# Kernel tuning notes

Measured on AMD Instinct MI355X. Metric: run time of the kernel, lower is better.

Reference implementation:

```python
import jax, jax.numpy as jnp
import numpy as np

C = 512
NH = 4
HD = C // NH
G = 32  # min(32, C) and C % 32 == 0
EPS = 1e-5


def setup_inputs() -> dict:
    key = jax.random.key(0)
    ks = jax.random.split(key, 11)
    s = 1.0 / np.sqrt(C)
    return {
        "x": jax.random.normal(ks[0], (16, C, 32, 32), dtype=jnp.float32),
        "gamma": jnp.ones((C,), jnp.float32),
        "beta": jnp.zeros((C,), jnp.float32),
        "wq": jax.random.normal(ks[1], (C, C), jnp.float32) * s,
        "bq": jax.random.normal(ks[2], (C,), jnp.float32) * 0.01,
        "wk": jax.random.normal(ks[3], (C, C), jnp.float32) * s,
        "bk": jax.random.normal(ks[4], (C,), jnp.float32) * 0.01,
        "wv": jax.random.normal(ks[5], (C, C), jnp.float32) * s,
        "bv": jax.random.normal(ks[6], (C,), jnp.float32) * 0.01,
        "wp": jax.random.normal(ks[7], (C, C), jnp.float32) * s,
        "bp": jax.random.normal(ks[8], (C,), jnp.float32) * 0.01,
    }


def _group_norm(x, gamma, beta):
    b, c, h, w = x.shape
    xr = x.reshape(b, G, c // G, h, w)
    mean = xr.mean(axis=(2, 3, 4), keepdims=True)
    var = xr.var(axis=(2, 3, 4), keepdims=True)
    xn = ((xr - mean) * jax.lax.rsqrt(var + EPS)).reshape(b, c, h, w)
    return xn * gamma[None, :, None, None] + beta[None, :, None, None]


def _conv1x1(x, w, b):
    # 1x1 conv == per-position channel GEMM
    return jnp.einsum('oc,bchw->bohw', w, x) + b[None, :, None, None]


def reference(x, gamma, beta, wq, bq, wk, bk, wv, bv, wp, bp):
    b, c, h, w = x.shape
    hw = h * w
    scale = HD ** (-0.5)
    hn = _group_norm(x, gamma, beta)
    q = _conv1x1(hn, wq, bq).reshape(b, NH, HD, hw)
    k = _conv1x1(hn, wk, bk).reshape(b, NH, HD, hw)
    v = _conv1x1(hn, wv, bv).reshape(b, NH, HD, hw)
    attn = jnp.einsum('bhdq,bhdk->bhqk', q, k) * scale  # [b, nh, hw, hw]
    attn = jax.nn.softmax(attn, axis=-1)
    out = jnp.einsum('bhqk,bhdk->bhdq', attn, v)  # [b, nh, hd, hw]
    out = out.reshape(b, c, h, w)
    out = _conv1x1(out, wp, bp)
    return x + out
```

## Files before the change

### kernel.cpp

```cpp
#include <hip/hip_runtime.h>
#include <math.h>

#define CCH 512
#define NH 4
#define HD 128
#define HW 1024
#define BATCH 16
#define EPS 1e-5f

typedef __attribute__((ext_vector_type(8))) short bfrag;
typedef __attribute__((ext_vector_type(4))) float f4;
typedef __attribute__((ext_vector_type(16))) float f16v;

static __device__ __forceinline__ unsigned short f2bf(float f) {
  union { float f; unsigned u; } v;
  v.f = f;
  unsigned r = v.u + 0x7fff + ((v.u >> 16) & 1);
  return (unsigned short)(r >> 16);
}
static __device__ __forceinline__ unsigned pack2(unsigned short a, unsigned short b) {
  return (unsigned)a | ((unsigned)b << 16);
}
static __device__ __forceinline__ void ldg_lds16(const unsigned short* g,
                                                 unsigned short* l) {
  __builtin_amdgcn_global_load_lds(
      (const __attribute__((address_space(1))) unsigned int*)g,
      (__attribute__((address_space(3))) unsigned int*)l, 16, 0, 0);
}

#define QSCALE 0.08838834764831845f

__global__ __launch_bounds__(256) void wcvt_kernel(const float* __restrict__ s0,
                                                   const float* __restrict__ s1,
                                                   const float* __restrict__ s2,
                                                   const float* __restrict__ s3,
                                                   unsigned short* __restrict__ d) {
  const float* srcs[4] = {s0, s1, s2, s3};
  const float* s = srcs[blockIdx.y];
  unsigned short* dp = d + (size_t)blockIdx.y * CCH * CCH;
  int i = blockIdx.x * 256 + threadIdx.x;
  f4 v = ((const f4*)s)[i];
  ushort4 o;
  o.x = f2bf(v.x); o.y = f2bf(v.y); o.z = f2bf(v.z); o.w = f2bf(v.w);
  ((ushort4*)dp)[i] = o;
}

__global__ __launch_bounds__(256) void gn_kernel(const float* __restrict__ x,
                                                 const float* __restrict__ gamma,
                                                 const float* __restrict__ beta,
                                                 unsigned short* __restrict__ hn) {
  int b = blockIdx.x >> 5, g = blockIdx.x & 31;
  const float* xp = x + ((size_t)b * CCH + g * 16) * HW;
  int t = threadIdx.x;
  float s = 0.f, ss = 0.f;
  const f4* xp4 = (const f4*)xp;
  for (int i = t; i < 4096; i += 256) {
    f4 v = xp4[i];
    s += v.x + v.y + v.z + v.w;
    ss += v.x * v.x + v.y * v.y + v.z * v.z + v.w * v.w;
  }
#pragma unroll
  for (int off = 32; off > 0; off >>= 1) {
    s += __shfl_xor(s, off);
    ss += __shfl_xor(ss, off);
  }
  __shared__ float rs[4], rss[4];
  int w = t >> 6;
  if ((t & 63) == 0) { rs[w] = s; rss[w] = ss; }
  __syncthreads();
  s = rs[0] + rs[1] + rs[2] + rs[3];
  ss = rss[0] + rss[1] + rss[2] + rss[3];
  const float invn = 1.f / (16 * HW);
  float mean = s * invn;
  float var = ss * invn - mean * mean;
  float rstd = rsqrtf(var + EPS);
  float a_[16], b_[16];
#pragma unroll
  for (int c = 0; c < 16; ++c) {
    float gm = gamma[g * 16 + c] * rstd;
    a_[c] = gm;
    b_[c] = beta[g * 16 + c] - mean * gm;
  }
#pragma unroll
  for (int i = 0; i < 4; ++i) {
    int p = t + 256 * i;
    unsigned short tv[16];
#pragma unroll
    for (int c = 0; c < 16; ++c) tv[c] = f2bf(xp[c * HW + p] * a_[c] + b_[c]);
    uint4 u0, u1;
    u0.x = pack2(tv[0], tv[1]);  u0.y = pack2(tv[2], tv[3]);
    u0.z = pack2(tv[4], tv[5]);  u0.w = pack2(tv[6], tv[7]);
    u1.x = pack2(tv[8], tv[9]);  u1.y = pack2(tv[10], tv[11]);
    u1.z = pack2(tv[12], tv[13]); u1.w = pack2(tv[14], tv[15]);
    unsigned short* dst = hn + ((size_t)b * HW + p) * CCH + g * 16;
    *(uint4*)dst = u0;
    *(uint4*)(dst + 8) = u1;
  }
}

template <int PROJ>
__global__ __launch_bounds__(256, 3) void mm_kernel(
    const unsigned short* __restrict__ Xt, const unsigned short* __restrict__ Wb,
    const float* __restrict__ b0, const float* __restrict__ b1,
    const float* __restrict__ b2, const float* __restrict__ resid,
    unsigned short* __restrict__ O0, unsigned short* __restrict__ O1,
    unsigned short* __restrict__ O2, float* __restrict__ Ofp) {
  int b = blockIdx.z;
  int p0 = blockIdx.x * 128;
  int c0g = blockIdx.y * 128;
  __shared__ __align__(16) unsigned short Xs[128 * 32];
  __shared__ __align__(16) unsigned short Ws[128 * 32];
  int t = threadIdx.x;
  int w = t >> 6, lane = t & 63, l15 = lane & 15, quad = lane >> 4;
  int wp = (w & 1) * 64, wc = (w >> 1) * 64;
  const unsigned short* Xb = Xt + (size_t)b * HW * CCH;
  const unsigned short* Wr = Wb + (size_t)c0g * CCH;
  f4 acc[4][4] = {};
  for (int k0 = 0; k0 < CCH; k0 += 32) {
    __syncthreads();
#pragma unroll
    for (int j = 0; j < 2; ++j) {
      int chk = w * 2 + j;
      int r = chk * 16 + (lane >> 2);
      int c = (lane & 3) ^ (r & 3);
      ldg_lds16(&Xb[(size_t)(p0 + r) * CCH + k0 + c * 8], &Xs[chk * 512]);
      ldg_lds16(&Wr[(size_t)r * CCH + k0 + c * 8], &Ws[chk * 512]);
    }
    __syncthreads();
    bfrag af[4], bf[4];
#pragma unroll
    for (int pt = 0; pt < 4; ++pt) {
      int r = wp + pt * 16 + l15;
      af[pt] = *(const bfrag*)&Xs[r * 32 + (quad ^ (r & 3)) * 8];
    }
#pragma unroll
    for (int ct = 0; ct < 4; ++ct) {
      int r = wc + ct * 16 + l15;
      bf[ct] = *(const bfrag*)&Ws[r * 32 + (quad ^ (r & 3)) * 8];
    }
#pragma unroll
    for (int pt = 0; pt < 4; ++pt)
#pragma unroll
      for (int ct = 0; ct < 4; ++ct)
        acc[pt][ct] = __builtin_amdgcn_mfma_f32_16x16x32_bf16(
            af[pt], bf[ct], acc[pt][ct], 0, 0, 0);
  }
  if (PROJ) {
#pragma unroll
    for (int ct = 0; ct < 4; ++ct) {
      int ch = c0g + wc + ct * 16 + l15;
      float bi = b0[ch];
#pragma unroll
      for (int pt = 0; pt < 4; ++pt) {
        int pos = p0 + wp + pt * 16 + quad * 4;
        f4 v = acc[pt][ct];
        size_t off = (size_t)b * CCH * HW + (size_t)ch * HW + pos;
        float4 rv = *(const float4*)&resid[off];
        float4 st;
        st.x = v.x + bi + rv.x; st.y = v.y + bi + rv.y;
        st.z = v.z + bi + rv.z; st.w = v.w + bi + rv.w;
        *(float4*)&Ofp[off] = st;
      }
    }
  } else {
    int mat = c0g >> 9;
    int c0 = c0g & 511;
    const float* bias = mat == 0 ? b0 : (mat == 1 ? b1 : b2);
    unsigned short* O = mat == 0 ? O0 : (mat == 1 ? O1 : O2);
    const float sc = (mat == 0) ? QSCALE : 1.0f;
#pragma unroll
    for (int ct = 0; ct < 4; ++ct) {
      int ch = c0 + wc + ct * 16 + l15;
      float bi = bias[ch];
#pragma unroll
      for (int pt = 0; pt < 4; ++pt) {
        int pos = p0 + wp + pt * 16 + quad * 4;
        f4 v = acc[pt][ct];
        if (mat < 2) {
          unsigned short* Op = O + (size_t)b * HW * CCH;
          Op[(size_t)(pos + 0) * CCH + ch] = f2bf((v.x + bi) * sc);
          Op[(size_t)(pos + 1) * CCH + ch] = f2bf((v.y + bi) * sc);
          Op[(size_t)(pos + 2) * CCH + ch] = f2bf((v.z + bi) * sc);
          Op[(size_t)(pos + 3) * CCH + ch] = f2bf((v.w + bi) * sc);
        } else {
          unsigned short* Op = O + (size_t)b * CCH * HW;
          ushort4 st;
          st.x = f2bf(v.x + bi); st.y = f2bf(v.y + bi);
          st.z = f2bf(v.z + bi); st.w = f2bf(v.w + bi);
          *(ushort4*)&Op[(size_t)ch * HW + pos] = st;
        }
      }
    }
  }
}

__global__ __launch_bounds__(512, 2) void attn_kernel(
    const unsigned short* __restrict__ Qt, const unsigned short* __restrict__ Kt,
    const unsigned short* __restrict__ Vc, unsigned short* __restrict__ Ot) {
  int bh = blockIdx.x;
  int b = bh >> 2, h = bh & 3;
  int q0 = blockIdx.y * 256;
  int t = threadIdx.x;
  int w = t >> 6, lane = t & 63;
  int l31 = lane & 31, half = lane >> 5;
  __shared__ __align__(16) unsigned short Ks[2][64 * 128];
  __shared__ __align__(16) unsigned short Vs[2][128 * 64];
  int q = q0 + w * 32 + l31;
  const unsigned short* Kbase = Kt + (size_t)b * HW * CCH + h * HD;
  const unsigned short* Vbase = Vc + ((size_t)b * CCH + h * HD) * HW;
  bfrag qf[8];
#pragma unroll
  for (int ks = 0; ks < 8; ++ks)
    qf[ks] = *(const bfrag*)&Qt[((size_t)b * HW + q) * CCH + h * HD +
                                ks * 16 + half * 8];
  f16v o[4] = {};
  float lrow = 0.f;
  auto stage = [&](int kt, int bi) {
    int kk0 = kt * 64;
#pragma unroll
    for (int j = 0; j < 2; ++j) {
      int chk = w * 2 + j;
      {
        int r = chk * 4 + (lane >> 4);
        int c = (lane & 15) ^ (r & 15);
        ldg_lds16(&Kbase[(size_t)(kk0 + r) * CCH + c * 8], &Ks[bi][chk * 512]);
      }
      {
        int r = chk * 8 + (lane >> 3);
        int c = (lane & 7) ^ (r & 7);
        ldg_lds16(&Vbase[(size_t)r * HW + kk0 + c * 8], &Vs[bi][chk * 512]);
      }
    }
  };
  stage(0, 0);
  for (int kt = 0; kt < 16; ++kt) {
    __syncthreads();
    if (kt < 15) stage(kt + 1, (kt + 1) & 1);
    const unsigned short* K_ = Ks[kt & 1];
    const unsigned short* V_ = Vs[kt & 1];
    f16v S[2] = {};
#pragma unroll
    for (int ks = 0; ks < 8; ++ks) {
      int c16 = ks * 2 + half;
#pragma unroll
      for (int mt = 0; mt < 2; ++mt) {
        int r = mt * 32 + l31;
        bfrag kf = *(const bfrag*)&K_[r * 128 + ((c16 ^ (r & 15)) << 3)];
        S[mt] = __builtin_amdgcn_mfma_f32_32x32x16_bf16(kf, qf[ks], S[mt],
                                                        0, 0, 0);
      }
    }
    unsigned pd[16];
    float sum = 0.f;
#pragma unroll
    for (int mt = 0; mt < 2; ++mt)
#pragma unroll
      for (int i = 0; i < 8; ++i) {
        float p0 = __expf(S[mt][2 * i]);
        float p1 = __expf(S[mt][2 * i + 1]);
        sum += p0 + p1;
        pd[mt * 8 + i] = pack2(f2bf(p0), f2bf(p1));
      }
    lrow += sum;
#pragma unroll
    for (int mt = 0; mt < 2; ++mt)
#pragma unroll
      for (int s = 0; s < 2; ++s) {
        int base = mt * 8 + s * 4;
        unsigned s0 = half ? pd[base + 0] : pd[base + 2];
        unsigned s1 = half ? pd[base + 1] : pd[base + 3];
        unsigned r0 = (unsigned)__shfl_xor((int)s0, 32);
        unsigned r1 = (unsigned)__shfl_xor((int)s1, 32);
        union { unsigned u[4]; bfrag f; } pf;
        pf.u[0] = half ? r0 : pd[base + 0];
        pf.u[1] = half ? r1 : pd[base + 1];
        pf.u[2] = half ? pd[base + 2] : r0;
        pf.u[3] = half ? pd[base + 3] : r1;
        int c8 = (mt * 2 + s) * 2 + half;
#pragma unroll
        for (int dt = 0; dt < 4; ++dt) {
          int r = dt * 32 + l31;
          bfrag vf = *(const bfrag*)&V_[r * 64 + ((c8 ^ (r & 7)) << 3)];
          o[dt] = __builtin_amdgcn_mfma_f32_32x32x16_bf16(vf, pf.f, o[dt],
                                                          0, 0, 0);
        }
      }
  }
  lrow += __shfl_xor(lrow, 32);
  float inv = 1.f / lrow;
  unsigned short* Op = Ot + ((size_t)b * HW + q) * CCH + h * HD;
#pragma unroll
  for (int dt = 0; dt < 4; ++dt)
#pragma unroll
    for (int rg = 0; rg < 4; ++rg) {
      int d = dt * 32 + rg * 8 + half * 4;
      ushort4 st;
      st.x = f2bf(o[dt][rg * 4 + 0] * inv);
      st.y = f2bf(o[dt][rg * 4 + 1] * inv);
      st.z = f2bf(o[dt][rg * 4 + 2] * inv);
      st.w = f2bf(o[dt][rg * 4 + 3] * inv);
      *(ushort4*)&Op[d] = st;
    }
}

extern "C" void kernel_launch(void* const* d_in, const int* in_sizes, int n_in,
                              void* d_out, int out_size, void* d_ws,
                              size_t ws_size, hipStream_t stream) {
  const float* x = (const float*)d_in[0];
  const float* gamma = (const float*)d_in[1];
  const float* beta = (const float*)d_in[2];
  const float* wq = (const float*)d_in[3];
  const float* bq = (const float*)d_in[4];
  const float* wk = (const float*)d_in[5];
  const float* bk = (const float*)d_in[6];
  const float* wv = (const float*)d_in[7];
  const float* bv = (const float*)d_in[8];
  const float* wp = (const float*)d_in[9];
  const float* bp = (const float*)d_in[10];

  const size_t TS = (size_t)BATCH * HW * CCH;
  unsigned short* wB = (unsigned short*)d_ws;
  unsigned short* hn = wB + (size_t)4 * CCH * CCH;
  unsigned short* Qt = hn + TS;
  unsigned short* Kt = Qt + TS;
  unsigned short* Vc = Kt + TS;
  unsigned short* Ot = hn;

  wcvt_kernel<<<dim3(256, 4), 256, 0, stream>>>(wq, wk, wv, wp, wB);
  gn_kernel<<<dim3(BATCH * 32), 256, 0, stream>>>(x, gamma, beta, hn);
  mm_kernel<0><<<dim3(8, 12, BATCH), 256, 0, stream>>>(
      hn, wB, bq, bk, bv, nullptr, Qt, Kt, Vc, nullptr);
  attn_kernel<<<dim3(64, 4), 512, 0, stream>>>(Qt, Kt, Vc, Ot);
  mm_kernel<1><<<dim3(8, 4, BATCH), 256, 0, stream>>>(
      Ot, wB + (size_t)3 * CCH * CCH, bp, bp, bp, x, nullptr, nullptr, nullptr,
      (float*)d_out);
}
```

Baseline: 232.3 us.

## Shrink attention blocks, use exp2 with folded log2e, hardware bf16 packing, setprio

The attention kernel now runs 256-thread blocks over 128 queries each, with twice as many blocks, so each wave stages twice as many K/V chunks. The softmax switches from exp to exp2 by folding log2(e) into the Q scale. It also splits the row-sum into four partial accumulators and converts to bf16 with the packed v_cvt_pk_bf16_f32 instruction instead of software rounding. s_setprio is raised around the MFMA loops to favour matrix issue. These changes aim to cut ALU work in the softmax, shorten dependency chains and improve scheduling. The trade-off is twice the K/V traffic per query, since each block reloads all keys for fewer queries.

```diff
diff --git a/kernel.cpp b/kernel.cpp
--- a/kernel.cpp
+++ b/kernel.cpp
@@ -21,6 +21,16 @@
 static __device__ __forceinline__ unsigned pack2(unsigned short a, unsigned short b) {
   return (unsigned)a | ((unsigned)b << 16);
 }
+static __device__ __forceinline__ unsigned cvt_pk_bf16(float a, float b) {
+  unsigned r;
+  asm("v_cvt_pk_bf16_f32 %0, %1, %2" : "=v"(r) : "v"(a), "v"(b));
+  return r;
+}
+#if defined(__has_builtin) && __has_builtin(__builtin_amdgcn_exp2f)
+#define EXP2(x) __builtin_amdgcn_exp2f(x)
+#else
+#define EXP2(x) __expf((x) * 0.6931471805599453f)
+#endif
 static __device__ __forceinline__ void ldg_lds16(const unsigned short* g,
                                                  unsigned short* l) {
   __builtin_amdgcn_global_load_lds(
@@ -28,7 +38,7 @@
       (__attribute__((address_space(3))) unsigned int*)l, 16, 0, 0);
 }
 
-#define QSCALE 0.08838834764831845f
+#define QSCALE (0.08838834764831845f * 1.4426950408889634f)
 
 __global__ __launch_bounds__(256) void wcvt_kernel(const float* __restrict__ s0,
                                                    const float* __restrict__ s1,
@@ -194,12 +204,12 @@
   }
 }
 
-__global__ __launch_bounds__(512, 2) void attn_kernel(
+__global__ __launch_bounds__(256, 2) void attn_kernel(
     const unsigned short* __restrict__ Qt, const unsigned short* __restrict__ Kt,
     const unsigned short* __restrict__ Vc, unsigned short* __restrict__ Ot) {
   int bh = blockIdx.x;
   int b = bh >> 2, h = bh & 3;
-  int q0 = blockIdx.y * 256;
+  int q0 = blockIdx.y * 128;
   int t = threadIdx.x;
   int w = t >> 6, lane = t & 63;
   int l31 = lane & 31, half = lane >> 5;
@@ -214,12 +224,12 @@
     qf[ks] = *(const bfrag*)&Qt[((size_t)b * HW + q) * CCH + h * HD +
                                 ks * 16 + half * 8];
   f16v o[4] = {};
-  float lrow = 0.f;
+  float ls[4] = {};
   auto stage = [&](int kt, int bi) {
     int kk0 = kt * 64;
 #pragma unroll
-    for (int j = 0; j < 2; ++j) {
-      int chk = w * 2 + j;
+    for (int j = 0; j < 4; ++j) {
+      int chk = w * 4 + j;
       {
         int r = chk * 4 + (lane >> 4);
         int c = (lane & 15) ^ (r & 15);
@@ -239,6 +249,7 @@
     const unsigned short* K_ = Ks[kt & 1];
     const unsigned short* V_ = Vs[kt & 1];
     f16v S[2] = {};
+    __builtin_amdgcn_s_setprio(1);
 #pragma unroll
     for (int ks = 0; ks < 8; ++ks) {
       int c16 = ks * 2 + half;
@@ -250,18 +261,17 @@
                                                         0, 0, 0);
       }
     }
+    __builtin_amdgcn_s_setprio(0);
     unsigned pd[16];
-    float sum = 0.f;
 #pragma unroll
     for (int mt = 0; mt < 2; ++mt)
 #pragma unroll
       for (int i = 0; i < 8; ++i) {
-        float p0 = __expf(S[mt][2 * i]);
-        float p1 = __expf(S[mt][2 * i + 1]);
-        sum += p0 + p1;
-        pd[mt * 8 + i] = pack2(f2bf(p0), f2bf(p1));
-      }
-    lrow += sum;
+        float p0 = EXP2(S[mt][2 * i]);
+        float p1 = EXP2(S[mt][2 * i + 1]);
+        ls[i & 3] += p0 + p1;
+        pd[mt * 8 + i] = cvt_pk_bf16(p0, p1);
+      }
 #pragma unroll
     for (int mt = 0; mt < 2; ++mt)
 #pragma unroll
@@ -277,6 +287,7 @@
         pf.u[2] = half ? pd[base + 2] : r0;
         pf.u[3] = half ? pd[base + 3] : r1;
         int c8 = (mt * 2 + s) * 2 + half;
+        __builtin_amdgcn_s_setprio(1);
 #pragma unroll
         for (int dt = 0; dt < 4; ++dt) {
           int r = dt * 32 + l31;
@@ -284,8 +295,10 @@
           o[dt] = __builtin_amdgcn_mfma_f32_32x32x16_bf16(vf, pf.f, o[dt],
                                                           0, 0, 0);
         }
-      }
-  }
+        __builtin_amdgcn_s_setprio(0);
+      }
+  }
+  float lrow = (ls[0] + ls[1]) + (ls[2] + ls[3]);
   lrow += __shfl_xor(lrow, 32);
   float inv = 1.f / lrow;
   unsigned short* Op = Ot + ((size_t)b * HW + q) * CCH + h * HD;
@@ -294,12 +307,10 @@
 #pragma unroll
     for (int rg = 0; rg < 4; ++rg) {
       int d = dt * 32 + rg * 8 + half * 4;
-      ushort4 st;
-      st.x = f2bf(o[dt][rg * 4 + 0] * inv);
-      st.y = f2bf(o[dt][rg * 4 + 1] * inv);
-      st.z = f2bf(o[dt][rg * 4 + 2] * inv);
-      st.w = f2bf(o[dt][rg * 4 + 3] * inv);
-      *(ushort4*)&Op[d] = st;
+      uint2 st;
+      st.x = cvt_pk_bf16(o[dt][rg * 4 + 0] * inv, o[dt][rg * 4 + 1] * inv);
+      st.y = cvt_pk_bf16(o[dt][rg * 4 + 2] * inv, o[dt][rg * 4 + 3] * inv);
+      *(uint2*)&Op[d] = st;
     }
 }
 
@@ -330,7 +341,7 @@
   gn_kernel<<<dim3(BATCH * 32), 256, 0, stream>>>(x, gamma, beta, hn);
   mm_kernel<0><<<dim3(8, 12, BATCH), 256, 0, stream>>>(
       hn, wB, bq, bk, bv, nullptr, Qt, Kt, Vc, nullptr);
-  attn_kernel<<<dim3(64, 4), 512, 0, stream>>>(Qt, Kt, Vc, Ot);
+  attn_kernel<<<dim3(64, 8), 256, 0, stream>>>(Qt, Kt, Vc, Ot);
   mm_kernel<1><<<dim3(8, 4, BATCH), 256, 0, stream>>>(
       Ot, wB + (size_t)3 * CCH * CCH, bp, bp, bp, x, nullptr, nullptr, nullptr,
       (float*)d_out);
```

New measurement: 222.6 us. 1.04x faster.
